# Optimization experiments

Measured on AMD Instinct MI355X. Metric: run time of the kernel, lower is better.

The kernel has to match this reference:

```python
import jax, jax.numpy as jnp
import numpy as np

DIM = 1024
HEADS = 16
HEAD_DIM = DIM // HEADS
EPS = 1e-5
THETA = 10000.0


def _rope(t):
    # t: (b, s, d). lucidrains rotary: interleaved pairs, full-dim rotation, theta=10000.
    b, s, d = t.shape
    inv_freq = 1.0 / (THETA ** (jnp.arange(0, d, 2, dtype=jnp.float32) / d))  # (d/2,)
    ang = jnp.arange(s, dtype=jnp.float32)[:, None] * inv_freq[None, :]        # (s, d/2)
    cos, sin = jnp.cos(ang), jnp.sin(ang)
    tp = t.reshape(b, s, d // 2, 2)
    x1, x2 = tp[..., 0], tp[..., 1]
    o1 = x1 * cos - x2 * sin
    o2 = x2 * cos + x1 * sin
    return jnp.stack([o1, o2], axis=-1).reshape(b, s, d)


def setup_inputs() -> dict:
    key = jax.random.key(0)
    ks = jax.random.split(key, 10)
    b, s, d = 2, 2048, DIM
    scale = 1.0 / np.sqrt(d)
    return {
        "x": jax.random.normal(ks[0], (b, s, d), dtype=jnp.float32),
        "mask": jax.random.normal(ks[1], (b, s, s), dtype=jnp.float32),
        "ln_g": jnp.ones((d,), dtype=jnp.float32),
        "ln_b": jnp.zeros((d,), dtype=jnp.float32),
        "w_qkv": jax.random.normal(ks[2], (3 * d, d), dtype=jnp.float32) * scale,
        "b_qkv": jnp.zeros((3 * d,), dtype=jnp.float32),
        "in_w": jax.random.normal(ks[3], (3 * d, d), dtype=jnp.float32) * scale,
        "in_b": jnp.zeros((3 * d,), dtype=jnp.float32),
        "out_w": jax.random.normal(ks[4], (d, d), dtype=jnp.float32) * scale,
        "out_b": jnp.zeros((d,), dtype=jnp.float32),
    }


def reference(x, mask, ln_g, ln_b, w_qkv, b_qkv, in_w, in_b, out_w, out_b):
    b, s, d = x.shape
    # LayerNorm
    mu = jnp.mean(x, axis=-1, keepdims=True)
    var = jnp.mean((x - mu) ** 2, axis=-1, keepdims=True)
    xn = (x - mu) * jax.lax.rsqrt(var + EPS) * ln_g + ln_b
    # fused qkv projection, then chunk
    qkv = xn @ w_qkv.T + b_qkv
    q, k, v = jnp.split(qkv, 3, axis=-1)
    # RoPE on q, k (full dim, interleaved pairs)
    q = _rope(q)
    k = _rope(k)
    # nn.MultiheadAttention re-applies its own in-projection
    wq, wk, wv = jnp.split(in_w, 3, axis=0)
    bq, bk, bv = jnp.split(in_b, 3, axis=0)
    def to_heads(t, w, bias):
        t = t @ w.T + bias
        return t.reshape(b, s, HEADS, HEAD_DIM).transpose(0, 2, 1, 3)  # (b,h,s,hd)
    qh = to_heads(q, wq, bq)
    kh = to_heads(k, wk, bk)
    vh = to_heads(v, wv, bv)
    scores = jnp.einsum('bhid,bhjd->bhij', qh, kh) / np.sqrt(HEAD_DIM)
    scores = scores + mask[:, None, :, :]  # mask repeated over heads
    attn = jax.nn.softmax(scores, axis=-1)
    out = jnp.einsum('bhij,bhjd->bhid', attn, vh)
    out = out.transpose(0, 2, 1, 3).reshape(b, s, d)
    return out @ out_w.T + out_b
```

## Files before the change

kernel.cpp:

```cpp
#include <hip/hip_runtime.h>

using u16 = unsigned short;
using u32 = unsigned int;
typedef __attribute__((ext_vector_type(8))) short short8;
typedef __attribute__((ext_vector_type(4))) float f32x4;

#define LOG2E 1.4426950408889634f
#define SCALE2 0.18033688011112042f

__device__ __forceinline__ u16 f2b(float f) {
  union { float f; unsigned u; } v; v.f = f;
  unsigned r = v.u + 0x7fffu + ((v.u >> 16) & 1u);
  return (u16)(r >> 16);
}

__device__ __forceinline__ void wg_barrier() {
  asm volatile("s_waitcnt lgkmcnt(0)\n\ts_barrier" ::: "memory");
}

__global__ __launch_bounds__(256) void prep(const float* __restrict__ w_qkv, u16* __restrict__ wqkv_b,
                                            const float* __restrict__ in_w, u16* __restrict__ inw_b,
                                            const float* __restrict__ out_w, u16* __restrict__ outw_b,
                                            float2* __restrict__ rtab,
                                            const float* __restrict__ mask, u16* __restrict__ maskp,
                                            const float* __restrict__ x,
                                            const float* __restrict__ ln_g,
                                            const float* __restrict__ ln_b,
                                            u16* __restrict__ xn) {
  __shared__ u16 T[128 * 68];
  __shared__ float sbuf[4], ssbuf[4];
  int blk = blockIdx.x, t = threadIdx.x;
  if (blk < 7168) {
    int i = blk * 256 + t;
    const float* s; u16* d; int off;
    if (i < 786432)       { s = w_qkv; d = wqkv_b; off = i; }
    else if (i < 1572864) { s = in_w;  d = inw_b;  off = i - 786432; }
    else                  { s = out_w; d = outw_b; off = i - 1572864; }
    float4 v = ((const float4*)s)[off];
    uint2 o;
    o.x = (unsigned)f2b(v.x) | ((unsigned)f2b(v.y) << 16);
    o.y = (unsigned)f2b(v.z) | ((unsigned)f2b(v.w) << 16);
    ((uint2*)d)[off] = o;
  } else if (blk < 11264) {
    int idx = (blk - 7168) * 256 + t;
    int pos = idx >> 9, i = idx & 511;
    float ifreq = exp2f(-(float)(2 * i) * (13.287712379549449f / 1024.0f));
    float ang = (float)pos * ifreq;
    rtab[idx] = make_float2(__cosf(ang), __sinf(ang));
  } else if (blk < 12288) {
    int mb = blk - 11264;
    int kt = mb & 31, qt = (mb >> 5) & 15, bb = mb >> 9;
    const float* src = mask + ((size_t)bb * 2048 + qt * 128) * 2048 + kt * 64;
    #pragma unroll
    for (int it = 0; it < 8; it++) {
      int id = it * 256 + t;
      int r = id >> 4, c4 = (id & 15) * 4;
      float4 v = *(const float4*)(src + (size_t)r * 2048 + c4);
      T[r * 68 + c4 + 0] = f2b(v.x * LOG2E);
      T[r * 68 + c4 + 1] = f2b(v.y * LOG2E);
      T[r * 68 + c4 + 2] = f2b(v.z * LOG2E);
      T[r * 68 + c4 + 3] = f2b(v.w * LOG2E);
    }
    __syncthreads();
    size_t obase = (size_t)(((bb * 16 + qt) * 32) + kt) * 8192;
    #pragma unroll
    for (int it = 0; it < 2; it++) {
      int pos = it * 256 + t;
      int l15 = pos & 15, g = pos >> 4;
      int w = g >> 3, p = (g >> 2) & 1, qd = g & 3;
      int qlocal = w * 32 + p * 16 + l15;
      u16 vals[16];
      #pragma unroll
      for (int mt = 0; mt < 4; mt++)
        #pragma unroll
        for (int reg = 0; reg < 4; reg++)
          vals[mt * 4 + reg] = T[qlocal * 68 + mt * 16 + qd * 4 + reg];
      uint4* dst = (uint4*)(maskp + obase + (size_t)pos * 16);
      dst[0] = *(uint4*)&vals[0];
      dst[1] = *(uint4*)&vals[8];
    }
  } else {
    int row = blk - 12288;
    const float* xr = x + (size_t)row * 1024;
    float4 v = *(const float4*)(xr + t * 4);
    float s = v.x + v.y + v.z + v.w;
    float ss = v.x * v.x + v.y * v.y + v.z * v.z + v.w * v.w;
    #pragma unroll
    for (int m = 1; m < 64; m <<= 1) {
      s  += __shfl_xor(s, m);
      ss += __shfl_xor(ss, m);
    }
    int wave = t >> 6, lane = t & 63;
    if (lane == 0) { sbuf[wave] = s; ssbuf[wave] = ss; }
    __syncthreads();
    s  = sbuf[0] + sbuf[1] + sbuf[2] + sbuf[3];
    ss = ssbuf[0] + ssbuf[1] + ssbuf[2] + ssbuf[3];
    float mean = s * (1.0f / 1024.0f);
    float var  = ss * (1.0f / 1024.0f) - mean * mean;
    float rstd = 1.0f / sqrtf(var + 1e-5f);
    float4 gv = *(const float4*)(ln_g + t * 4);
    float4 bv = *(const float4*)(ln_b + t * 4);
    uint2 o;
    o.x = (unsigned)f2b((v.x - mean) * rstd * gv.x + bv.x) |
          ((unsigned)f2b((v.y - mean) * rstd * gv.y + bv.y) << 16);
    o.y = (unsigned)f2b((v.z - mean) * rstd * gv.z + bv.z) |
          ((unsigned)f2b((v.w - mean) * rstd * gv.w + bv.w) << 16);
    *(uint2*)(xn + (size_t)row * 1024 + t * 4) = o;
  }
}

template<bool SLAB, bool OUT_BF16, bool ROPE, bool WVT>
__global__ __launch_bounds__(256, 3) void gemm_pipe(const u16* __restrict__ A, int lda,
                                                    const u16* __restrict__ W,
                                                    const float* __restrict__ bias,
                                                    const float2* __restrict__ rtab,
                                                    float* __restrict__ Cf,
                                                    u16* __restrict__ Cb,
                                                    u16* __restrict__ vT,
                                                    int ldc, int K) {
  __shared__ u16 As[2][128 * 36];
  __shared__ u16 Bs[2][128 * 36];
  int n0 = blockIdx.x * 128, m0 = blockIdx.y * 128;
  int aoff = SLAB ? ((n0 >> 10) << 10) : 0;
  int tid = threadIdx.x;
  int lane = tid & 63, l15 = lane & 15, quad = lane >> 4;
  int w = tid >> 6, mw = w & 1, nw = w >> 1;
  const u16* Abase = A + (size_t)m0 * lda + aoff;
  const u16* Wbase = W + (size_t)n0 * K;
  int r0 = tid >> 2;
  int c4 = (tid & 3) * 8;
  f32x4 acc[4][4];
  #pragma unroll
  for (int i = 0; i < 4; i++)
    #pragma unroll
    for (int j = 0; j < 4; j++) acc[i][j] = (f32x4){0.f, 0.f, 0.f, 0.f};

  uint4 a0, a1, w0, w1;
  uint4 b0, b1, x0, x1;
  #define GLOADS_A(k0)                                                        \
    a0 = *(const uint4*)(Abase + (size_t)(r0)      * lda + (k0) + c4);        \
    a1 = *(const uint4*)(Abase + (size_t)(r0 + 64) * lda + (k0) + c4);        \
    w0 = *(const uint4*)(Wbase + (size_t)(r0)      * K   + (k0) + c4);        \
    w1 = *(const uint4*)(Wbase + (size_t)(r0 + 64) * K   + (k0) + c4);
  #define GLOADS_B(k0)                                                        \
    b0 = *(const uint4*)(Abase + (size_t)(r0)      * lda + (k0) + c4);        \
    b1 = *(const uint4*)(Abase + (size_t)(r0 + 64) * lda + (k0) + c4);        \
    x0 = *(const uint4*)(Wbase + (size_t)(r0)      * K   + (k0) + c4);        \
    x1 = *(const uint4*)(Wbase + (size_t)(r0 + 64) * K   + (k0) + c4);
  #define LSTORES_A(bf)                                                       \
    *(uint4*)&As[bf][(r0)      * 36 + c4] = a0;                               \
    *(uint4*)&As[bf][(r0 + 64) * 36 + c4] = a1;                               \
    *(uint4*)&Bs[bf][(r0)      * 36 + c4] = w0;                               \
    *(uint4*)&Bs[bf][(r0 + 64) * 36 + c4] = w1;
  #define LSTORES_B(bf)                                                       \
    *(uint4*)&As[bf][(r0)      * 36 + c4] = b0;                               \
    *(uint4*)&As[bf][(r0 + 64) * 36 + c4] = b1;                               \
    *(uint4*)&Bs[bf][(r0)      * 36 + c4] = x0;                               \
    *(uint4*)&Bs[bf][(r0 + 64) * 36 + c4] = x1;
  #define COMPUTE(bf)                                                         \
    {                                                                         \
      short8 af[4], bfr[4];                                                   \
      _Pragma("unroll")                                                       \
      for (int mt = 0; mt < 4; mt++)                                          \
        af[mt] = *(const short8*)&As[bf][(mw * 64 + mt * 16 + l15) * 36 + quad * 8]; \
      _Pragma("unroll")                                                       \
      for (int nt = 0; nt < 4; nt++)                                          \
        bfr[nt] = *(const short8*)&Bs[bf][(nw * 64 + nt * 16 + l15) * 36 + quad * 8]; \
      _Pragma("unroll")                                                       \
      for (int mt = 0; mt < 4; mt++)                                          \
        _Pragma("unroll")                                                     \
        for (int nt = 0; nt < 4; nt++)                                        \
          acc[mt][nt] = __builtin_amdgcn_mfma_f32_16x16x32_bf16(              \
              af[mt], bfr[nt], acc[mt][nt], 0, 0, 0);                         \
    }

  GLOADS_A(0);
  LSTORES_A(0);
  GLOADS_A(32);
  GLOADS_B(64);
  wg_barrier();
  for (int k0 = 0; k0 < K; k0 += 64) {
    if (k0 + 32 < K)  { LSTORES_A(1); }
    if (k0 + 96 < K)  { GLOADS_A(k0 + 96); }
    COMPUTE(0);
    wg_barrier();
    if (k0 + 64 < K)  { LSTORES_B(0); }
    if (k0 + 128 < K) { GLOADS_B(k0 + 128); }
    COMPUTE(1);
    wg_barrier();
  }
  #undef GLOADS_A
  #undef GLOADS_B
  #undef LSTORES_A
  #undef LSTORES_B
  #undef COMPUTE
  int mb = m0 + mw * 64, nb = n0 + nw * 64;
  float bv[4];
  #pragma unroll
  for (int nt = 0; nt < 4; nt++) bv[nt] = bias[nb + nt * 16 + l15];
  #pragma unroll
  for (int mt = 0; mt < 4; mt++)
    #pragma unroll
    for (int nt = 0; nt < 4; nt++) {
      int col = nb + nt * 16 + l15;
      if (WVT && col >= 2048) {
        int hh = (col - 2048) >> 6, dd = (col - 2048) & 63;
        int row0 = mb + mt * 16 + quad * 4;
        int bbi = row0 >> 11, s0 = row0 & 2047;
        u16 vv[4];
        #pragma unroll
        for (int reg = 0; reg < 4; reg++) vv[reg] = f2b(acc[mt][nt][reg] + bv[nt]);
        *(uint2*)&vT[((size_t)((bbi * 16 + hh) * 64 + dd)) * 2048 + s0] = *(uint2*)vv;
      } else {
        #pragma unroll
        for (int reg = 0; reg < 4; reg++) {
          int row = mb + mt * 16 + quad * 4 + reg;
          float val = acc[mt][nt][reg] + bv[nt];
          if (ROPE && col < 2048) {
            float pr = __shfl_xor(val, 1);
            float2 cs = rtab[(size_t)(row & 2047) * 512 + ((col & 1023) >> 1)];
            val = (col & 1) ? fmaf(val, cs.x, pr * cs.y)
                            : fmaf(val, cs.x, -pr * cs.y);
          }
          if (OUT_BF16) Cb[(size_t)row * ldc + col] = f2b(val);
          else          Cf[(size_t)row * ldc + col] = val;
        }
      }
    }
}

__global__ __launch_bounds__(256) void attn_mfma(const u16* __restrict__ qkv2,
                                                 const u16* __restrict__ vT,
                                                 const u16* __restrict__ maskp,
                                                 u16* __restrict__ attn_out) {
  __shared__ u16 Kb[2][64 * 72];
  __shared__ u16 Vb[2][64 * 72];
  __shared__ u16 Ps[128 * 72];
  int h = blockIdx.x, qt = blockIdx.y, bb = blockIdx.z;
  int tid = threadIdx.x;
  int lane = tid & 63, l15 = lane & 15, quad = lane >> 4;
  int w = tid >> 6;
  int sr = tid >> 2, sc = (tid & 3) * 16;
  const u16* kslab = qkv2 + ((size_t)bb * 2048) * 3072 + 1024 + h * 64;
  const u16* vslab = vT + ((size_t)((bb * 16 + h) * 64)) * 2048;

  {
    int r = w * 32 + (lane >> 1), c0 = (lane & 1) * 32;
    const u16* src = qkv2 + (size_t)(bb * 2048 + qt * 128 + r) * 3072 + h * 64 + c0;
    #pragma unroll
    for (int u = 0; u < 4; u++)
      *(uint4*)&Ps[r * 72 + c0 + u * 8] = *(const uint4*)(src + u * 8);
  }
  {
    const u16* ks = kslab + (size_t)sr * 3072 + sc;
    const u16* vs = vslab + (size_t)sr * 2048 + sc;
    *(uint4*)&Kb[0][sr * 72 + sc]     = *(const uint4*)ks;
    *(uint4*)&Kb[0][sr * 72 + sc + 8] = *(const uint4*)(ks + 8);
    *(uint4*)&Vb[0][sr * 72 + sc]     = *(const uint4*)vs;
    *(uint4*)&Vb[0][sr * 72 + sc + 8] = *(const uint4*)(vs + 8);
  }
  short8 bq[2][2];
  #pragma unroll
  for (int p = 0; p < 2; p++)
    #pragma unroll
    for (int hk = 0; hk < 2; hk++)
      bq[p][hk] = *(const short8*)&Ps[(w * 32 + p * 16 + l15) * 72 + hk * 32 + quad * 8];
  float lsum[2] = {0.f, 0.f};
  f32x4 acc[2][4];
  #pragma unroll
  for (int p = 0; p < 2; p++)
    #pragma unroll
    for (int dt = 0; dt < 4; dt++) acc[p][dt] = (f32x4){0.f, 0.f, 0.f, 0.f};
  const u16* mtile = maskp + ((size_t)((bb * 16 + qt) * 32)) * 8192
                     + (((w * 2) * 4 + quad) * 16 + l15) * 16;
  wg_barrier();

  for (int kt = 0; kt < 32; kt++) {
    int b = kt & 1;
    uint4 mA[2], mB[2];
    {
      const u16* mt_ = mtile + (size_t)kt * 8192;
      #pragma unroll
      for (int p = 0; p < 2; p++) {
        const uint4* mq = (const uint4*)(mt_ + p * 1024);
        mA[p] = mq[0]; mB[p] = mq[1];
      }
    }
    uint4 kr0, kr1, vr0, vr1;
    if (kt + 1 < 32) {
      const u16* ks = kslab + (size_t)((kt + 1) * 64 + sr) * 3072 + sc;
      const u16* vs = vslab + (size_t)sr * 2048 + (kt + 1) * 64 + sc;
      kr0 = *(const uint4*)ks; kr1 = *(const uint4*)(ks + 8);
      vr0 = *(const uint4*)vs; vr1 = *(const uint4*)(vs + 8);
    }
    short8 ak[4][2];
    #pragma unroll
    for (int mt = 0; mt < 4; mt++)
      #pragma unroll
      for (int hk = 0; hk < 2; hk++)
        ak[mt][hk] = *(const short8*)&Kb[b][(mt * 16 + l15) * 72 + hk * 32 + quad * 8];
    #pragma unroll
    for (int p = 0; p < 2; p++) {
      f32x4 st[4];
      #pragma unroll
      for (int mt = 0; mt < 4; mt++) {
        f32x4 z = (f32x4){0.f, 0.f, 0.f, 0.f};
        z = __builtin_amdgcn_mfma_f32_16x16x32_bf16(ak[mt][0], bq[p][0], z, 0, 0, 0);
        st[mt] = __builtin_amdgcn_mfma_f32_16x16x32_bf16(ak[mt][1], bq[p][1], z, 0, 0, 0);
      }
      u32 wds[8] = {mA[p].x, mA[p].y, mA[p].z, mA[p].w, mB[p].x, mB[p].y, mB[p].z, mB[p].w};
      float mv[16];
      #pragma unroll
      for (int j = 0; j < 8; j++) {
        mv[2 * j]     = __uint_as_float(wds[j] << 16);
        mv[2 * j + 1] = __uint_as_float(wds[j] & 0xffff0000u);
      }
      int prow = (w * 32 + p * 16 + l15) * 72 + quad * 4;
      #pragma unroll
      for (int mt = 0; mt < 4; mt++) {
        u32 pk0, pk1;
        float sv0 = fmaf(st[mt][0], SCALE2, mv[mt * 4 + 0]);
        float sv1 = fmaf(st[mt][1], SCALE2, mv[mt * 4 + 1]);
        float sv2 = fmaf(st[mt][2], SCALE2, mv[mt * 4 + 2]);
        float sv3 = fmaf(st[mt][3], SCALE2, mv[mt * 4 + 3]);
        float p0 = __builtin_amdgcn_exp2f(sv0), p1 = __builtin_amdgcn_exp2f(sv1);
        float p2 = __builtin_amdgcn_exp2f(sv2), p3 = __builtin_amdgcn_exp2f(sv3);
        lsum[p] += (p0 + p1) + (p2 + p3);
        pk0 = ((__float_as_uint(p0) + 0x8000u) >> 16) |
              ((__float_as_uint(p1) + 0x8000u) & 0xffff0000u);
        pk1 = ((__float_as_uint(p2) + 0x8000u) >> 16) |
              ((__float_as_uint(p3) + 0x8000u) & 0xffff0000u);
        *(uint2*)&Ps[prow + mt * 16] = make_uint2(pk0, pk1);
      }
    }
    short8 ap[2][2];
    #pragma unroll
    for (int p = 0; p < 2; p++)
      #pragma unroll
      for (int hk = 0; hk < 2; hk++)
        ap[p][hk] = *(const short8*)&Ps[(w * 32 + p * 16 + l15) * 72 + hk * 32 + quad * 8];
    #pragma unroll
    for (int dt = 0; dt < 4; dt++) {
      short8 bv0 = *(const short8*)&Vb[b][(dt * 16 + l15) * 72 + quad * 8];
      short8 bv1 = *(const short8*)&Vb[b][(dt * 16 + l15) * 72 + 32 + quad * 8];
      #pragma unroll
      for (int p = 0; p < 2; p++) {
        acc[p][dt] = __builtin_amdgcn_mfma_f32_16x16x32_bf16(ap[p][0], bv0, acc[p][dt], 0, 0, 0);
        acc[p][dt] = __builtin_amdgcn_mfma_f32_16x16x32_bf16(ap[p][1], bv1, acc[p][dt], 0, 0, 0);
      }
    }
    if (kt + 1 < 32) {
      int nb = b ^ 1;
      *(uint4*)&Kb[nb][sr * 72 + sc]     = kr0;
      *(uint4*)&Kb[nb][sr * 72 + sc + 8] = kr1;
      *(uint4*)&Vb[nb][sr * 72 + sc]     = vr0;
      *(uint4*)&Vb[nb][sr * 72 + sc + 8] = vr1;
    }
    wg_barrier();
  }
  #pragma unroll
  for (int p = 0; p < 2; p++) {
    float l = lsum[p];
    l += __shfl_xor(l, 16);
    l += __shfl_xor(l, 32);
    #pragma unroll
    for (int reg = 0; reg < 4; reg++) {
      float lq = __shfl(l, quad * 4 + reg);
      float inv = 1.0f / lq;
      int grow = bb * 2048 + qt * 128 + w * 32 + p * 16 + quad * 4 + reg;
      #pragma unroll
      for (int dt = 0; dt < 4; dt++)
        attn_out[(size_t)grow * 1024 + h * 64 + dt * 16 + l15] = f2b(acc[p][dt][reg] * inv);
    }
  }
}

extern "C" void kernel_launch(void* const* d_in, const int* in_sizes, int n_in,
                              void* d_out, int out_size, void* d_ws, size_t ws_size,
                              hipStream_t stream) {
  const float* x     = (const float*)d_in[0];
  const float* mask  = (const float*)d_in[1];
  const float* ln_g  = (const float*)d_in[2];
  const float* ln_b  = (const float*)d_in[3];
  const float* w_qkv = (const float*)d_in[4];
  const float* b_qkv = (const float*)d_in[5];
  const float* in_w  = (const float*)d_in[6];
  const float* in_b  = (const float*)d_in[7];
  const float* out_w = (const float*)d_in[8];
  const float* out_b = (const float*)d_in[9];
  float* out = (float*)d_out;
  char* ws = (char*)d_ws;

  u16* wqkv_b = (u16*)(ws);
  u16* inw_b  = (u16*)(ws + 6291456ull);
  u16* outw_b = (u16*)(ws + 12582912ull);
  u16* xn_b   = (u16*)(ws + 14680064ull);
  u16* attn_b = xn_b;
  u16* qkv_b  = (u16*)(ws + 23068672ull);
  u16* qkv2_b = (u16*)(ws + 48234496ull);
  float2* rtab = (float2*)qkv2_b;
  u16* vT     = (u16*)(ws + 73400320ull);
  u16* maskp  = (u16*)(ws + 81788928ull);

  prep<<<16384, 256, 0, stream>>>(w_qkv, wqkv_b, in_w, inw_b, out_w, outw_b,
                                  rtab, mask, maskp, x, ln_g, ln_b, xn_b);
  gemm_pipe<false, true, true, false><<<dim3(24, 32), 256, 0, stream>>>(
      xn_b, 1024, wqkv_b, b_qkv, rtab, nullptr, qkv_b, nullptr, 3072, 1024);
  gemm_pipe<true, true, false, true><<<dim3(24, 32), 256, 0, stream>>>(
      qkv_b, 3072, inw_b, in_b, nullptr, nullptr, qkv2_b, vT, 3072, 1024);
  attn_mfma<<<dim3(16, 16, 2), 256, 0, stream>>>(qkv2_b, vT, maskp, attn_b);
  gemm_pipe<false, false, false, false><<<dim3(8, 32), 256, 0, stream>>>(
      attn_b, 1024, outw_b, out_b, nullptr, out, nullptr, nullptr, 1024, 1024);
}
```

Baseline: 304.0 us.

## Split attention work across 8 waves per block and prefetch mask tiles

The attention kernel now runs 512 threads (8 waves) per block, so each wave handles 16 query rows instead of 32. This halves per-thread registers and raises latency hiding. Each thread now loads a single 16-byte chunk of K/V instead of two. The mask tile is software-prefetched one iteration ahead alongside K/V. Probabilities are packed to bf16 with a hardware cvt_pk instruction instead of manual rounding. The cost is that K/V fragments read from LDS are now shared by twice as many waves, so LDS read traffic per MFMA goes up and barriers synchronise more waves.

```diff
diff --git a/kernel.cpp b/kernel.cpp
--- a/kernel.cpp
+++ b/kernel.cpp
@@ -229,10 +229,10 @@
     }
 }
 
-__global__ __launch_bounds__(256) void attn_mfma(const u16* __restrict__ qkv2,
-                                                 const u16* __restrict__ vT,
-                                                 const u16* __restrict__ maskp,
-                                                 u16* __restrict__ attn_out) {
+__global__ __launch_bounds__(512, 4) void attn_mfma(const u16* __restrict__ qkv2,
+                                                    const u16* __restrict__ vT,
+                                                    const u16* __restrict__ maskp,
+                                                    u16* __restrict__ attn_out) {
   __shared__ u16 Kb[2][64 * 72];
   __shared__ u16 Vb[2][64 * 72];
   __shared__ u16 Ps[128 * 72];
@@ -240,58 +240,45 @@
   int tid = threadIdx.x;
   int lane = tid & 63, l15 = lane & 15, quad = lane >> 4;
   int w = tid >> 6;
-  int sr = tid >> 2, sc = (tid & 3) * 16;
+  int sr = tid >> 3, sc = (tid & 7) * 8;
   const u16* kslab = qkv2 + ((size_t)bb * 2048) * 3072 + 1024 + h * 64;
   const u16* vslab = vT + ((size_t)((bb * 16 + h) * 64)) * 2048;
 
   {
-    int r = w * 32 + (lane >> 1), c0 = (lane & 1) * 32;
+    int r = tid >> 2, c0 = (tid & 3) * 16;
     const u16* src = qkv2 + (size_t)(bb * 2048 + qt * 128 + r) * 3072 + h * 64 + c0;
-    #pragma unroll
-    for (int u = 0; u < 4; u++)
-      *(uint4*)&Ps[r * 72 + c0 + u * 8] = *(const uint4*)(src + u * 8);
+    *(uint4*)&Ps[r * 72 + c0]     = *(const uint4*)src;
+    *(uint4*)&Ps[r * 72 + c0 + 8] = *(const uint4*)(src + 8);
   }
   {
-    const u16* ks = kslab + (size_t)sr * 3072 + sc;
-    const u16* vs = vslab + (size_t)sr * 2048 + sc;
-    *(uint4*)&Kb[0][sr * 72 + sc]     = *(const uint4*)ks;
-    *(uint4*)&Kb[0][sr * 72 + sc + 8] = *(const uint4*)(ks + 8);
-    *(uint4*)&Vb[0][sr * 72 + sc]     = *(const uint4*)vs;
-    *(uint4*)&Vb[0][sr * 72 + sc + 8] = *(const uint4*)(vs + 8);
-  }
-  short8 bq[2][2];
-  #pragma unroll
-  for (int p = 0; p < 2; p++)
-    #pragma unroll
-    for (int hk = 0; hk < 2; hk++)
-      bq[p][hk] = *(const short8*)&Ps[(w * 32 + p * 16 + l15) * 72 + hk * 32 + quad * 8];
-  float lsum[2] = {0.f, 0.f};
-  f32x4 acc[2][4];
-  #pragma unroll
-  for (int p = 0; p < 2; p++)
-    #pragma unroll
-    for (int dt = 0; dt < 4; dt++) acc[p][dt] = (f32x4){0.f, 0.f, 0.f, 0.f};
+    *(uint4*)&Kb[0][sr * 72 + sc] = *(const uint4*)(kslab + (size_t)sr * 3072 + sc);
+    *(uint4*)&Vb[0][sr * 72 + sc] = *(const uint4*)(vslab + (size_t)sr * 2048 + sc);
+  }
+  short8 bq[2];
+  #pragma unroll
+  for (int hk = 0; hk < 2; hk++)
+    bq[hk] = *(const short8*)&Ps[(w * 16 + l15) * 72 + hk * 32 + quad * 8];
+  float lsum = 0.f;
+  f32x4 acc[4];
+  #pragma unroll
+  for (int dt = 0; dt < 4; dt++) acc[dt] = (f32x4){0.f, 0.f, 0.f, 0.f};
   const u16* mtile = maskp + ((size_t)((bb * 16 + qt) * 32)) * 8192
-                     + (((w * 2) * 4 + quad) * 16 + l15) * 16;
+                     + ((w * 4 + quad) * 16 + l15) * 16;
+  uint4 mA, mB;
+  {
+    const uint4* mq = (const uint4*)mtile;
+    mA = mq[0]; mB = mq[1];
+  }
   wg_barrier();
 
   for (int kt = 0; kt < 32; kt++) {
     int b = kt & 1;
-    uint4 mA[2], mB[2];
-    {
-      const u16* mt_ = mtile + (size_t)kt * 8192;
-      #pragma unroll
-      for (int p = 0; p < 2; p++) {
-        const uint4* mq = (const uint4*)(mt_ + p * 1024);
-        mA[p] = mq[0]; mB[p] = mq[1];
-      }
-    }
-    uint4 kr0, kr1, vr0, vr1;
+    uint4 kr, vr, mAn, mBn;
     if (kt + 1 < 32) {
-      const u16* ks = kslab + (size_t)((kt + 1) * 64 + sr) * 3072 + sc;
-      const u16* vs = vslab + (size_t)sr * 2048 + (kt + 1) * 64 + sc;
-      kr0 = *(const uint4*)ks; kr1 = *(const uint4*)(ks + 8);
-      vr0 = *(const uint4*)vs; vr1 = *(const uint4*)(vs + 8);
+      kr = *(const uint4*)(kslab + (size_t)((kt + 1) * 64 + sr) * 3072 + sc);
+      vr = *(const uint4*)(vslab + (size_t)sr * 2048 + (kt + 1) * 64 + sc);
+      const uint4* mq = (const uint4*)(mtile + (size_t)(kt + 1) * 8192);
+      mAn = mq[0]; mBn = mq[1];
     }
     short8 ak[4][2];
     #pragma unroll
@@ -299,78 +286,66 @@
       #pragma unroll
       for (int hk = 0; hk < 2; hk++)
         ak[mt][hk] = *(const short8*)&Kb[b][(mt * 16 + l15) * 72 + hk * 32 + quad * 8];
-    #pragma unroll
-    for (int p = 0; p < 2; p++) {
-      f32x4 st[4];
-      #pragma unroll
-      for (int mt = 0; mt < 4; mt++) {
-        f32x4 z = (f32x4){0.f, 0.f, 0.f, 0.f};
-        z = __builtin_amdgcn_mfma_f32_16x16x32_bf16(ak[mt][0], bq[p][0], z, 0, 0, 0);
-        st[mt] = __builtin_amdgcn_mfma_f32_16x16x32_bf16(ak[mt][1], bq[p][1], z, 0, 0, 0);
-      }
-      u32 wds[8] = {mA[p].x, mA[p].y, mA[p].z, mA[p].w, mB[p].x, mB[p].y, mB[p].z, mB[p].w};
-      float mv[16];
-      #pragma unroll
-      for (int j = 0; j < 8; j++) {
-        mv[2 * j]     = __uint_as_float(wds[j] << 16);
-        mv[2 * j + 1] = __uint_as_float(wds[j] & 0xffff0000u);
-      }
-      int prow = (w * 32 + p * 16 + l15) * 72 + quad * 4;
-      #pragma unroll
-      for (int mt = 0; mt < 4; mt++) {
-        u32 pk0, pk1;
-        float sv0 = fmaf(st[mt][0], SCALE2, mv[mt * 4 + 0]);
-        float sv1 = fmaf(st[mt][1], SCALE2, mv[mt * 4 + 1]);
-        float sv2 = fmaf(st[mt][2], SCALE2, mv[mt * 4 + 2]);
-        float sv3 = fmaf(st[mt][3], SCALE2, mv[mt * 4 + 3]);
-        float p0 = __builtin_amdgcn_exp2f(sv0), p1 = __builtin_amdgcn_exp2f(sv1);
-        float p2 = __builtin_amdgcn_exp2f(sv2), p3 = __builtin_amdgcn_exp2f(sv3);
-        lsum[p] += (p0 + p1) + (p2 + p3);
-        pk0 = ((__float_as_uint(p0) + 0x8000u) >> 16) |
-              ((__float_as_uint(p1) + 0x8000u) & 0xffff0000u);
-        pk1 = ((__float_as_uint(p2) + 0x8000u) >> 16) |
-              ((__float_as_uint(p3) + 0x8000u) & 0xffff0000u);
-        *(uint2*)&Ps[prow + mt * 16] = make_uint2(pk0, pk1);
-      }
-    }
-    short8 ap[2][2];
-    #pragma unroll
-    for (int p = 0; p < 2; p++)
-      #pragma unroll
-      for (int hk = 0; hk < 2; hk++)
-        ap[p][hk] = *(const short8*)&Ps[(w * 32 + p * 16 + l15) * 72 + hk * 32 + quad * 8];
+    f32x4 st[4];
+    #pragma unroll
+    for (int mt = 0; mt < 4; mt++) {
+      f32x4 z = (f32x4){0.f, 0.f, 0.f, 0.f};
+      z = __builtin_amdgcn_mfma_f32_16x16x32_bf16(ak[mt][0], bq[0], z, 0, 0, 0);
+      st[mt] = __builtin_amdgcn_mfma_f32_16x16x32_bf16(ak[mt][1], bq[1], st[mt] = z, 0, 0, 0);
+    }
+    u32 wds[8] = {mA.x, mA.y, mA.z, mA.w, mB.x, mB.y, mB.z, mB.w};
+    float mv[16];
+    #pragma unroll
+    for (int j = 0; j < 8; j++) {
+      mv[2 * j]     = __uint_as_float(wds[j] << 16);
+      mv[2 * j + 1] = __uint_as_float(wds[j] & 0xffff0000u);
+    }
+    int prow = (w * 16 + l15) * 72 + quad * 4;
+    #pragma unroll
+    for (int mt = 0; mt < 4; mt++) {
+      float sv0 = fmaf(st[mt][0], SCALE2, mv[mt * 4 + 0]);
+      float sv1 = fmaf(st[mt][1], SCALE2, mv[mt * 4 + 1]);
+      float sv2 = fmaf(st[mt][2], SCALE2, mv[mt * 4 + 2]);
+      float sv3 = fmaf(st[mt][3], SCALE2, mv[mt * 4 + 3]);
+      float p0 = __builtin_amdgcn_exp2f(sv0), p1 = __builtin_amdgcn_exp2f(sv1);
+      float p2 = __builtin_amdgcn_exp2f(sv2), p3 = __builtin_amdgcn_exp2f(sv3);
+      lsum += (p0 + p1) + (p2 + p3);
+      u32 pk0, pk1;
+      asm("v_cvt_pk_bf16_f32 %0, %1, %2" : "=v"(pk0) : "v"(p0), "v"(p1));
+      asm("v_cvt_pk_bf16_f32 %0, %1, %2" : "=v"(pk1) : "v"(p2), "v"(p3));
+      *(uint2*)&Ps[prow + mt * 16] = make_uint2(pk0, pk1);
+    }
+    short8 ap[2];
+    #pragma unroll
+    for (int hk = 0; hk < 2; hk++)
+      ap[hk] = *(const short8*)&Ps[(w * 16 + l15) * 72 + hk * 32 + quad * 8];
     #pragma unroll
     for (int dt = 0; dt < 4; dt++) {
       short8 bv0 = *(const short8*)&Vb[b][(dt * 16 + l15) * 72 + quad * 8];
       short8 bv1 = *(const short8*)&Vb[b][(dt * 16 + l15) * 72 + 32 + quad * 8];
-      #pragma unroll
-      for (int p = 0; p < 2; p++) {
-        acc[p][dt] = __builtin_amdgcn_mfma_f32_16x16x32_bf16(ap[p][0], bv0, acc[p][dt], 0, 0, 0);
-        acc[p][dt] = __builtin_amdgcn_mfma_f32_16x16x32_bf16(ap[p][1], bv1, acc[p][dt], 0, 0, 0);
-      }
+      acc[dt] = __builtin_amdgcn_mfma_f32_16x16x32_bf16(ap[0], bv0, acc[dt], 0, 0, 0);
+      acc[dt] = __builtin_amdgcn_mfma_f32_16x16x32_bf16(ap[1], bv1, acc[dt], 0, 0, 0);
     }
     if (kt + 1 < 32) {
       int nb = b ^ 1;
-      *(uint4*)&Kb[nb][sr * 72 + sc]     = kr0;
-      *(uint4*)&Kb[nb][sr * 72 + sc + 8] = kr1;
-      *(uint4*)&Vb[nb][sr * 72 + sc]     = vr0;
-      *(uint4*)&Vb[nb][sr * 72 + sc + 8] = vr1;
+      *(uint4*)&Kb[nb][sr * 72 + sc] = kr;
+      *(uint4*)&Vb[nb][sr * 72 + sc] = vr;
+      mA = mAn; mB = mBn;
     }
     wg_barrier();
   }
-  #pragma unroll
-  for (int p = 0; p < 2; p++) {
-    float l = lsum[p];
+  {
+    float l = lsum;
     l += __shfl_xor(l, 16);
     l += __shfl_xor(l, 32);
     #pragma unroll
     for (int reg = 0; reg < 4; reg++) {
       float lq = __shfl(l, quad * 4 + reg);
       float inv = 1.0f / lq;
-      int grow = bb * 2048 + qt * 128 + w * 32 + p * 16 + quad * 4 + reg;
+      int grow = bb * 2048 + qt * 128 + w * 16 + quad * 4 + reg;
       #pragma unroll
       for (int dt = 0; dt < 4; dt++)
-        attn_out[(size_t)grow * 1024 + h * 64 + dt * 16 + l15] = f2b(acc[p][dt][reg] * inv);
+        attn_out[(size_t)grow * 1024 + h * 64 + dt * 16 + l15] = f2b(acc[dt][reg] * inv);
     }
   }
 }
@@ -408,7 +383,7 @@
       xn_b, 1024, wqkv_b, b_qkv, rtab, nullptr, qkv_b, nullptr, 3072, 1024);
   gemm_pipe<true, true, false, true><<<dim3(24, 32), 256, 0, stream>>>(
       qkv_b, 3072, inw_b, in_b, nullptr, nullptr, qkv2_b, vT, 3072, 1024);
-  attn_mfma<<<dim3(16, 16, 2), 256, 0, stream>>>(qkv2_b, vT, maskp, attn_b);
+  attn_mfma<<<dim3(16, 16, 2), 512, 0, stream>>>(qkv2_b, vT, maskp, attn_b);
   gemm_pipe<false, false, false, false><<<dim3(8, 32), 256, 0, stream>>>(
       attn_b, 1024, outw_b, out_b, nullptr, out, nullptr, nullptr, 1024, 1024);
 }
```

After: 303.4 us. About the same (-0.2%).
